# Kernel optimization log

Measured on AMD Instinct MI355X. Metric: run time of the kernel, lower is better.

Reference implementation:

```python
import math
import jax, jax.numpy as jnp
import numpy as np

DIM = 1024
NUM_HEADS = 16
HEAD_DIM = DIM // NUM_HEADS


def setup_inputs() -> dict:
    key = jax.random.key(0)
    ks = jax.random.split(key, 5)
    b, t, d = 2, 2048, DIM
    x = jax.random.normal(ks[0], (b, t, d), dtype=jnp.float32)
    mask = jnp.ones((b, t), dtype=jnp.float32)  # 1 = keep, 0 = pad
    s_in = 1.0 / math.sqrt(d)
    w_qkv = jax.random.normal(ks[1], (3 * d, d), dtype=jnp.float32) * s_in
    b_qkv = jnp.zeros((3 * d,), dtype=jnp.float32)
    w_out = jax.random.normal(ks[2], (d, d), dtype=jnp.float32) * s_in
    b_out = jnp.zeros((d,), dtype=jnp.float32)
    return {"x": x, "mask": mask, "w_qkv": w_qkv, "b_qkv": b_qkv,
            "w_out": w_out, "b_out": b_out}


def reference(x, mask, w_qkv, b_qkv, w_out, b_out):
    b, t, d = x.shape
    h, hd = NUM_HEADS, HEAD_DIM
    # qkv projection (torch Linear: x @ W^T + b)
    qkv = x @ w_qkv.T + b_qkv                          # [b,t,3d]
    q, k, v = jnp.split(qkv, 3, axis=-1)
    def reshape(z):
        return z.reshape(b, t, h, hd).transpose(0, 2, 1, 3)  # [b,h,t,hd]
    q, k, v = reshape(q), reshape(k), reshape(v)
    att = jnp.einsum('bhqd,bhkd->bhqk', q, k) / math.sqrt(hd)  # [b,h,t,t]
    causal = jnp.tril(jnp.ones((t, t), dtype=bool))            # [t,t]
    keep = causal[None, None, :, :] & (mask[:, None, None, :] != 0)
    att = jnp.where(keep, att, -jnp.inf)
    att = jax.nn.softmax(att, axis=-1)
    out = jnp.einsum('bhqk,bhkd->bhqd', att, v)        # [b,h,t,hd]
    out = out.transpose(0, 2, 1, 3).reshape(b, t, d)
    return out @ w_out.T + b_out
```

## Files before the change

kernel.cpp:

```cpp
#include <hip/hip_runtime.h>
#include <cmath>

#define B_ 2
#define T_ 2048
#define D_ 1024
#define H_ 16
#define HD_ 64
#define M_ (B_ * T_)
#define N3_ (3 * D_)
#define K_ 1024

typedef _Float16 halfx8 __attribute__((ext_vector_type(8)));
typedef _Float16 halfx4 __attribute__((ext_vector_type(4)));
typedef _Float16 halfx2 __attribute__((ext_vector_type(2)));
typedef __fp16 fp16x2 __attribute__((ext_vector_type(2)));
typedef float f32x4 __attribute__((ext_vector_type(4)));
typedef float f32x16 __attribute__((ext_vector_type(16)));

#define ASYNC_COPY16(gp, lp) \
  __builtin_amdgcn_global_load_lds((__attribute__((address_space(1))) void*)(gp), \
      (__attribute__((address_space(3))) void*)(lp), 16, 0, 0)

#define QSCALE 0.1803368801111204f
#define RTHR 4.0f

__device__ __forceinline__ float exp2fast(float x) {
#if __has_builtin(__builtin_amdgcn_exp2f)
    return __builtin_amdgcn_exp2f(x);
#else
    return exp2f(x);
#endif
}

__device__ const int QT2_OF[24] = {15,15,7, 14,14, 13,13,6, 12,12, 11,11,5, 10,10, 9,9,4, 8,8, 3,2,1,0};
__device__ const int C2_OF[24]  = { 0, 1,0,  0, 1,  0, 1,0,  0, 1,  0, 1,0,  0, 1, 0,1,0,  0,1, 0,0,0,0};

__global__ __launch_bounds__(256) void prep_all(
    const float* __restrict__ x, const float* __restrict__ wq,
    const float* __restrict__ wo, const float* __restrict__ mask,
    _Float16* __restrict__ xh, _Float16* __restrict__ wqh,
    _Float16* __restrict__ woh, float* __restrict__ kbias,
    int* __restrict__ tflags)
{
    int bid = blockIdx.x;
    if (bid >= 4096) {
        int i = (bid - 4096) * 256 + threadIdx.x;
        float mv = mask[i];
        kbias[i] = (mv != 0.f) ? 0.f : -INFINITY;
        unsigned long long bal = __ballot(mv != 0.f);
        if ((threadIdx.x & 63) == 0) tflags[i >> 6] = (bal == ~0ULL) ? 1 : 0;
        return;
    }
    const float* s; _Float16* d; int off;
    if (bid < 2048)      { s = x;  d = xh;  off = bid; }
    else if (bid < 3584) { s = wq; d = wqh; off = bid - 2048; }
    else                 { s = wo; d = woh; off = bid - 3584; }
    int i = (off * 256 + threadIdx.x) * 8;
    float4 a = *(const float4*)(s + i);
    float4 b = *(const float4*)(s + i + 4);
    halfx8 h;
    h[0] = (_Float16)a.x; h[1] = (_Float16)a.y; h[2] = (_Float16)a.z; h[3] = (_Float16)a.w;
    h[4] = (_Float16)b.x; h[5] = (_Float16)b.y; h[6] = (_Float16)b.z; h[7] = (_Float16)b.w;
    *(halfx8*)(d + i) = h;
}

__global__ __launch_bounds__(256) void gemm_qkv(
    const _Float16* __restrict__ A, const _Float16* __restrict__ Wt,
    const float* __restrict__ bias,
    _Float16* __restrict__ qh, _Float16* __restrict__ kh, _Float16* __restrict__ vth)
{
    __shared__ _Float16 As[128 * 32];
    __shared__ _Float16 Bs[128 * 32];
    const int tid = threadIdx.x;
    const int lane = tid & 63, w = tid >> 6;
    const int col = lane & 15, quad = lane >> 4;
    const int wr = w >> 1, wc = w & 1;
    const int m0 = blockIdx.y << 7, n0 = blockIdx.x << 7;

    const int c0 = w * 2, c1 = c0 + 1;
    const int r0 = c0 * 16 + (lane >> 2), r1 = c1 * 16 + (lane >> 2);
    const int ks = (lane & 3) << 3;

    f32x4 acc[4][4] = {};

    for (int k0 = 0; k0 < K_; k0 += 32) {
        ASYNC_COPY16(A  + (size_t)(m0 + r0) * K_ + k0 + ks, &As[c0 * 512]);
        ASYNC_COPY16(A  + (size_t)(m0 + r1) * K_ + k0 + ks, &As[c1 * 512]);
        ASYNC_COPY16(Wt + (size_t)(n0 + r0) * K_ + k0 + ks, &Bs[c0 * 512]);
        ASYNC_COPY16(Wt + (size_t)(n0 + r1) * K_ + k0 + ks, &Bs[c1 * 512]);
        __syncthreads();
        halfx8 af[4], bf[4];
#pragma unroll
        for (int i = 0; i < 4; ++i)
            af[i] = *(const halfx8*)&As[(wr * 64 + i * 16 + col) * 32 + quad * 8];
#pragma unroll
        for (int j = 0; j < 4; ++j)
            bf[j] = *(const halfx8*)&Bs[(wc * 64 + j * 16 + col) * 32 + quad * 8];
#pragma unroll
        for (int i = 0; i < 4; ++i)
#pragma unroll
            for (int j = 0; j < 4; ++j)
                acc[i][j] = __builtin_amdgcn_mfma_f32_16x16x32_f16(af[i], bf[j], acc[i][j], 0, 0, 0);
        __syncthreads();
    }

#pragma unroll
    for (int i = 0; i < 4; ++i) {
#pragma unroll
        for (int r = 0; r < 4; ++r) {
            int m = m0 + wr * 64 + i * 16 + quad * 4 + r;
            int bb = m >> 11, tt = m & (T_ - 1);
#pragma unroll
            for (int j = 0; j < 4; ++j) {
                int n = n0 + wc * 64 + j * 16 + col;
                float val = acc[i][j][r] + bias[n];
                int which = n >> 10, head = (n >> 6) & 15, dd = n & 63;
                if (which == 0) {
                    qh[((size_t)(bb * H_ + head) * T_ + tt) * HD_ + dd] = (_Float16)(val * QSCALE);
                } else if (which == 1) {
                    int hi = ((dd >> 3) ^ (tt & 7) ^ ((tt >> 3) & 7)) & 7;
                    int dds = (hi << 3) | (dd & 7);
                    kh[((size_t)(bb * H_ + head) * T_ + tt) * HD_ + dds] = (_Float16)val;
                } else {
                    int hi = (((tt >> 3) & 7) ^ (dd & 7) ^ ((dd >> 3) & 7)) & 7;
                    int tts = (tt & ~63) | (hi << 3) | (tt & 7);
                    vth[((size_t)(bb * H_ + head) * HD_ + dd) * T_ + tts] = (_Float16)val;
                }
            }
        }
    }
}

__global__ __launch_bounds__(256) void gemm_out(
    const _Float16* __restrict__ A, const _Float16* __restrict__ Wt,
    const float* __restrict__ bias, float* __restrict__ C)
{
    __shared__ _Float16 As[2][128 * 32];
    __shared__ _Float16 Bs[2][64 * 32];
    const int tid = threadIdx.x;
    const int lane = tid & 63, w = tid >> 6;
    const int col = lane & 15, quad = lane >> 4;
    const int m0 = blockIdx.y << 7, n0 = blockIdx.x << 6;

    const int c0 = w * 2, c1 = c0 + 1;
    const int rA0 = c0 * 16 + (lane >> 2), rA1 = c1 * 16 + (lane >> 2);
    const int rB = w * 16 + (lane >> 2);
    const int ks = (lane & 3) << 3;

    f32x4 acc[2][4] = {};

    for (int k0 = 0; k0 < K_; k0 += 64) {
        ASYNC_COPY16(A  + (size_t)(m0 + rA0) * K_ + k0 + ks,      &As[0][c0 * 512]);
        ASYNC_COPY16(A  + (size_t)(m0 + rA1) * K_ + k0 + ks,      &As[0][c1 * 512]);
        ASYNC_COPY16(A  + (size_t)(m0 + rA0) * K_ + k0 + 32 + ks, &As[1][c0 * 512]);
        ASYNC_COPY16(A  + (size_t)(m0 + rA1) * K_ + k0 + 32 + ks, &As[1][c1 * 512]);
        ASYNC_COPY16(Wt + (size_t)(n0 + rB) * K_ + k0 + ks,       &Bs[0][w * 512]);
        ASYNC_COPY16(Wt + (size_t)(n0 + rB) * K_ + k0 + 32 + ks,  &Bs[1][w * 512]);
        __syncthreads();
#pragma unroll
        for (int half = 0; half < 2; ++half) {
            halfx8 af[2], bf[4];
#pragma unroll
            for (int i = 0; i < 2; ++i)
                af[i] = *(const halfx8*)&As[half][(w * 32 + i * 16 + col) * 32 + quad * 8];
#pragma unroll
            for (int j = 0; j < 4; ++j)
                bf[j] = *(const halfx8*)&Bs[half][(j * 16 + col) * 32 + quad * 8];
#pragma unroll
            for (int i = 0; i < 2; ++i)
#pragma unroll
                for (int j = 0; j < 4; ++j)
                    acc[i][j] = __builtin_amdgcn_mfma_f32_16x16x32_f16(af[i], bf[j], acc[i][j], 0, 0, 0);
        }
        __syncthreads();
    }

#pragma unroll
    for (int i = 0; i < 2; ++i) {
#pragma unroll
        for (int r = 0; r < 4; ++r) {
            int m = m0 + w * 32 + i * 16 + quad * 4 + r;
#pragma unroll
            for (int j = 0; j < 4; ++j) {
                int n = n0 + j * 16 + col;
                C[(size_t)m * D_ + n] = acc[i][j][r] + bias[n];
            }
        }
    }
}

__global__ __launch_bounds__(256, 3) void attn_kernel(
    const _Float16* __restrict__ qh, const _Float16* __restrict__ kh,
    const _Float16* __restrict__ vth, const float* __restrict__ kbias,
    const int* __restrict__ tflags,
    float* __restrict__ pm, float* __restrict__ pl,
    _Float16* __restrict__ po, _Float16* __restrict__ oh)
{
    __shared__ _Float16 Ks[2][64 * 64];
    __shared__ _Float16 Vt[2][64 * 64];

    const int item = blockIdx.x >> 5;
    const int qt = QT2_OF[item], c = C2_OF[item];
    const int hb = blockIdx.x & 31;
    const int h = hb & 15, b = hb >> 4;
    const bool split = (qt >= 8);
    const int tid = threadIdx.x;
    const int lane = tid & 63, w = tid >> 6;
    const int l31 = lane & 31, q2 = lane >> 5;

    const int kt0 = (split && c) ? (qt + 1) : 0;
    const int ktend = (split && !c) ? qt : (2 * qt + 1);

    const int bh = b * H_ + h;
    const _Float16* qp = qh + (size_t)bh * T_ * HD_;
    const _Float16* kp = kh + (size_t)bh * T_ * HD_;
    const _Float16* vp = vth + (size_t)bh * HD_ * T_;
    const float* kb = kbias + (size_t)b * T_;
    const int* tf = tflags + b * 32;

    const int qbase = qt * 128 + w * 32;
    const int q_row = qbase + l31;

    halfx8 bq[4];
#pragma unroll
    for (int hc = 0; hc < 4; ++hc)
        bq[hc] = *(const halfx8*)(qp + (size_t)q_row * HD_ + hc * 16 + q2 * 8);

    float mrow = -INFINITY;
    float lrow = 0.f;
    f32x16 oacc[2] = {};
    const fp16x2 one2 = {(__fp16)1.f, (__fp16)1.f};

    {
        const _Float16* ksrc = kp + (size_t)(kt0 * 64 + w * 16) * HD_;
        ASYNC_COPY16(ksrc + lane * 8, &Ks[0][(w * 16) * 64]);
        ASYNC_COPY16(ksrc + 8 * HD_ + lane * 8, &Ks[0][(w * 16 + 8) * 64]);
        const _Float16* vsrc = vp + (size_t)(w * 16 + (lane >> 3)) * T_
                                 + kt0 * 64 + (lane & 7) * 8;
        ASYNC_COPY16(vsrc, &Vt[0][(w * 16) * 64]);
        ASYNC_COPY16(vsrc + 8 * T_, &Vt[0][(w * 16 + 8) * 64]);
    }

    for (int kt = kt0; kt <= ktend; ++kt) {
        const int cur = (kt - kt0) & 1;
        __syncthreads();
        if (kt < ktend) {
            const int nb = cur ^ 1;
            const _Float16* ksrc = kp + (size_t)((kt + 1) * 64 + w * 16) * HD_;
            ASYNC_COPY16(ksrc + lane * 8, &Ks[nb][(w * 16) * 64]);
            ASYNC_COPY16(ksrc + 8 * HD_ + lane * 8, &Ks[nb][(w * 16 + 8) * 64]);
            const _Float16* vsrc = vp + (size_t)(w * 16 + (lane >> 3)) * T_
                                     + (kt + 1) * 64 + (lane & 7) * 8;
            ASYNC_COPY16(vsrc, &Vt[nb][(w * 16) * 64]);
            ASYNC_COPY16(vsrc + 8 * T_, &Vt[nb][(w * 16 + 8) * 64]);
        }
        if (kt * 64 > qbase + 31) continue;

        const int allkeep = tf[kt];
        const int kb2max = (qbase + 31 - kt * 64 >= 32) ? 2 : 1;

        auto qk_half = [&](int kb2v) -> f32x16 {
            f32x16 a = {};
#pragma unroll
            for (int hc = 0; hc < 4; ++hc) {
                int seg = (hc * 2 + q2) ^ (l31 & 7) ^ ((kb2v * 4 + (l31 >> 3)) & 7);
                halfx8 ka = *(const halfx8*)&Ks[cur][(kb2v * 32 + l31) * 64 + seg * 8];
                a = __builtin_amdgcn_mfma_f32_32x32x16_f16(ka, bq[hc], a, 0, 0, 0);
            }
            return a;
        };
        f32x16 sa0, sa1;
        __builtin_amdgcn_s_setprio(1);
        sa0 = qk_half(0);
        if (kb2max == 2) sa1 = qk_half(1);
        __builtin_amdgcn_s_setprio(0);

        auto smpv = [&](const f32x16& a, int kb2v) {
            float t0 = fmaxf(fmaxf(a[0],  a[1]),  a[2]);
            float t1 = fmaxf(fmaxf(a[3],  a[4]),  a[5]);
            float t2 = fmaxf(fmaxf(a[6],  a[7]),  a[8]);
            float t3 = fmaxf(fmaxf(a[9],  a[10]), a[11]);
            float t4 = fmaxf(fmaxf(a[12], a[13]), a[14]);
            float u0 = fmaxf(fmaxf(t0, t1), t2);
            float u1 = fmaxf(fmaxf(t3, t4), a[15]);
            float mx = fmaxf(u0, u1);

            if (__any(mx > mrow + RTHR)) {
                float mxo = fmaxf(mx, __shfl_xor(mx, 32, 64));
                float mnew = fmaxf(mrow, mxo);
                float alpha = exp2fast(mrow - mnew);
                lrow *= alpha;
#pragma unroll
                for (int db = 0; db < 2; ++db)
#pragma unroll
                    for (int r = 0; r < 16; ++r) oacc[db][r] *= alpha;
                mrow = mnew;
            }

            const bool fastk = allkeep && (kt * 64 + kb2v * 32 + 31 <= qbase);
            halfx4 pf[4];
            float s0 = 0.f, s1 = 0.f;
            if (fastk) {
#pragma unroll
                for (int cc = 0; cc < 4; ++cc) {
                    float e0 = exp2fast(a[cc * 4 + 0] - mrow);
                    float e1 = exp2fast(a[cc * 4 + 1] - mrow);
                    float e2 = exp2fast(a[cc * 4 + 2] - mrow);
                    float e3 = exp2fast(a[cc * 4 + 3] - mrow);
                    fp16x2 lo = __builtin_amdgcn_cvt_pkrtz(e0, e1);
                    fp16x2 hi = __builtin_amdgcn_cvt_pkrtz(e2, e3);
                    halfx2* pfv = (halfx2*)&pf[cc];
                    pfv[0] = __builtin_bit_cast(halfx2, lo);
                    pfv[1] = __builtin_bit_cast(halfx2, hi);
#if __has_builtin(__builtin_amdgcn_fdot2)
                    s0 = __builtin_amdgcn_fdot2(lo, one2, s0, false);
                    s1 = __builtin_amdgcn_fdot2(hi, one2, s1, false);
#else
                    s0 += e0 + e1; s1 += e2 + e3;
#endif
                }
            } else {
#pragma unroll
                for (int cc = 0; cc < 4; ++cc) {
                    float e[4];
#pragma unroll
                    for (int j = 0; j < 4; ++j) {
                        int key = kt * 64 + kb2v * 32 + 8 * cc + 4 * q2 + j;
                        float add = allkeep ? 0.f : kb[key];
                        e[j] = (key <= q_row) ? exp2fast(a[cc * 4 + j] + add - mrow) : 0.f;
                    }
                    fp16x2 lo = __builtin_amdgcn_cvt_pkrtz(e[0], e[1]);
                    fp16x2 hi = __builtin_amdgcn_cvt_pkrtz(e[2], e[3]);
                    halfx2* pfv = (halfx2*)&pf[cc];
                    pfv[0] = __builtin_bit_cast(halfx2, lo);
                    pfv[1] = __builtin_bit_cast(halfx2, hi);
#if __has_builtin(__builtin_amdgcn_fdot2)
                    s0 = __builtin_amdgcn_fdot2(lo, one2, s0, false);
                    s1 = __builtin_amdgcn_fdot2(hi, one2, s1, false);
#else
                    s0 += e[0] + e[1]; s1 += e[2] + e[3];
#endif
                }
            }
            lrow += s0 + s1;

            __builtin_amdgcn_s_setprio(1);
#pragma unroll
            for (int db = 0; db < 2; ++db)
#pragma unroll
                for (int cc = 0; cc < 4; ++cc) {
                    int ck = kb2v * 4 + cc;
                    int seg = ck ^ (l31 & 7) ^ ((db * 4 + (l31 >> 3)) & 7);
                    halfx4 va = *(const halfx4*)&Vt[cur][(db * 32 + l31) * 64 + seg * 8 + q2 * 4];
                    oacc[db] = __builtin_amdgcn_mfma_f32_32x32x8f16(va, pf[cc], oacc[db], 0, 0, 0);
                }
            __builtin_amdgcn_s_setprio(0);
        };

        smpv(sa0, 0);
        if (kb2max == 2) smpv(sa1, 1);
    }

    lrow += __shfl_xor(lrow, 32, 64);

    const int qloc = w * 32 + l31;
    _Float16* ohrow = oh + ((size_t)(b * T_ + qt * 128 + qloc)) * D_ + h * 64;

    if (!split) {
        const float linv = 1.f / lrow;
#pragma unroll
        for (int db = 0; db < 2; ++db)
#pragma unroll
            for (int gg = 0; gg < 4; ++gg) {
                halfx4 ov;
#pragma unroll
                for (int j = 0; j < 4; ++j)
                    ov[j] = (_Float16)(oacc[db][gg * 4 + j] * linv);
                *(halfx4*)(ohrow + db * 32 + 8 * gg + 4 * q2) = ov;
            }
    } else {
        const int slot = (bh * 8 + (qt - 8)) * 2 + c;
        if (q2 == 0) {
            pm[(size_t)slot * 128 + qloc] = mrow;
            pl[(size_t)slot * 128 + qloc] = lrow;
        }
        _Float16* pob = (c == 0) ? ohrow
                      : po + ((size_t)(bh * 8 + (qt - 8)) * 128 + qloc) * 64;
#pragma unroll
        for (int db = 0; db < 2; ++db)
#pragma unroll
            for (int gg = 0; gg < 4; ++gg) {
                halfx4 ov;
#pragma unroll
                for (int j = 0; j < 4; ++j)
                    ov[j] = (_Float16)(oacc[db][gg * 4 + j]);
                *(halfx4*)(pob + db * 32 + 8 * gg + 4 * q2) = ov;
            }
    }
}

__global__ __launch_bounds__(256) void attn_combine(
    const float* __restrict__ pm, const float* __restrict__ pl,
    const _Float16* __restrict__ po, _Float16* __restrict__ oh)
{
    const int qi = blockIdx.x;
    const int h = blockIdx.y, b = blockIdx.z;
    const int bh = b * H_ + h;
    const int tid = threadIdx.x;
    const int r = tid >> 1, dh = tid & 1;

    const int s0 = (bh * 8 + qi) * 2;
    float m0 = pm[(size_t)s0 * 128 + r],       m1 = pm[(size_t)(s0 + 1) * 128 + r];
    float l0 = pl[(size_t)s0 * 128 + r],       l1 = pl[(size_t)(s0 + 1) * 128 + r];
    float ms = fmaxf(m0, m1);
    float w0 = exp2f(m0 - ms), w1 = exp2f(m1 - ms);
    float linv = 1.f / (w0 * l0 + w1 * l1);
    w0 *= linv; w1 *= linv;

    _Float16* ohrow = oh + ((size_t)(b * T_ + (qi + 8) * 128 + r)) * D_ + h * 64 + dh * 32;
    const _Float16* src = po + ((size_t)(bh * 8 + qi) * 128 + r) * 64 + dh * 32;

#pragma unroll
    for (int g = 0; g < 4; ++g) {
        halfx8 o0 = *(const halfx8*)(ohrow + g * 8);
        halfx8 o1 = *(const halfx8*)(src + g * 8);
        halfx8 ov;
#pragma unroll
        for (int j = 0; j < 8; ++j)
            ov[j] = (_Float16)(w0 * (float)o0[j] + w1 * (float)o1[j]);
        *(halfx8*)(ohrow + g * 8) = ov;
    }
}

extern "C" void kernel_launch(void* const* d_in, const int* in_sizes, int n_in,
                              void* d_out, int out_size, void* d_ws, size_t ws_size,
                              hipStream_t stream)
{
    (void)in_sizes; (void)n_in; (void)out_size; (void)ws_size;
    const float* x     = (const float*)d_in[0];
    const float* mask  = (const float*)d_in[1];
    const float* w_qkv = (const float*)d_in[2];
    const float* b_qkv = (const float*)d_in[3];
    const float* w_out = (const float*)d_in[4];
    const float* b_out = (const float*)d_in[5];
    float* out = (float*)d_out;

    const size_t QKV1 = (size_t)B_ * H_ * T_ * HD_;
    _Float16* xh  = (_Float16*)d_ws;
    _Float16* wqh = xh  + (size_t)M_ * K_;
    _Float16* woh = wqh + (size_t)N3_ * K_;
    _Float16* qh  = woh + (size_t)D_ * K_;
    _Float16* kh  = qh  + QKV1;
    _Float16* vth = kh  + QKV1;
    _Float16* oh  = vth + QKV1;
    _Float16* po  = oh  + QKV1;
    float* kbias  = (float*)(po + (size_t)32 * 8 * 128 * 64);
    float* pm     = kbias + (size_t)B_ * T_;
    float* pl     = pm + (size_t)32 * 16 * 128;
    int* tflags   = (int*)(pl + (size_t)32 * 16 * 128);

    prep_all<<<4112, 256, 0, stream>>>(x, w_qkv, w_out, mask,
                                       xh, wqh, woh, kbias, tflags);
    gemm_qkv<<<dim3(N3_ / 128, M_ / 128), 256, 0, stream>>>(
        xh, wqh, b_qkv, qh, kh, vth);
    attn_kernel<<<dim3(768, 1, 1), 256, 0, stream>>>(
        qh, kh, vth, kbias, tflags, pm, pl, po, oh);
    attn_combine<<<dim3(8, H_, B_), 256, 0, stream>>>(
        pm, pl, po, oh);
    gemm_out<<<dim3(D_ / 64, M_ / 128), 256, 0, stream>>>(
        oh, woh, b_out, out);
}
```

Before: 181.7 us.

## Split causal attention KV range into up to three chunks per query tile

Replaces the two-way KV split for the upper query tiles with a table-driven schedule of 37 work items, in which query tiles 3 and up are split into two or three KV chunks of roughly equal length. The combine kernel is extended to merge two or three partial results using their stored max and sum statistics. The aim is to balance per-block work better and give the 256-CU device more blocks in flight. The cost is more partial writes and reads, a heavier combine kernel, and extra per-block table lookups.

```diff
diff --git a/kernel.cpp b/kernel.cpp
--- a/kernel.cpp
+++ b/kernel.cpp
@@ -32,8 +32,22 @@
 #endif
 }
 
-__device__ const int QT2_OF[24] = {15,15,7, 14,14, 13,13,6, 12,12, 11,11,5, 10,10, 9,9,4, 8,8, 3,2,1,0};
-__device__ const int C2_OF[24]  = { 0, 1,0,  0, 1,  0, 1,0,  0, 1,  0, 1,0,  0, 1, 0,1,0,  0,1, 0,0,0,0};
+#define NITEM 37
+#define NPO 21
+__device__ const int QT3_[NITEM] = {
+    15,15, 15,14,14,14,13, 13,13,12,12, 12,11,11,11,10,7,7,
+    10,10,9,9,6,6, 9,8,8,8,5,5,2, 4,4, 3,3,1, 0};
+__device__ const int KT0_[NITEM] = {
+    0,11, 22,0,10,20,0, 10,19,0,9, 18,0,8,16,0,0,8,
+    8,15,0,7,0,7, 14,0,6,12,0,6,0, 0,5, 0,4,0, 0};
+__device__ const int KTE_[NITEM] = {
+    10,21, 31,9,19,29,9, 18,27,8,17, 25,7,15,23,7,7,15,
+    14,21,6,13,6,13, 19,5,11,17,5,11,5, 4,9, 3,7,3, 1};
+__device__ const int C3_[NITEM] = {
+    0,1, 2,0,1,2,0, 1,2,0,1, 2,0,1,2,0,0,1,
+    1,2,0,1,0,1, 2,0,1,2,0,1,0, 0,1, 0,1,0, 0};
+__device__ const int SLOT_BASE[16] = {0,1,2,3,5,7,9,11,13,16,19,22,25,28,31,34};
+__device__ const int PO_BASE[16]   = {0,0,0,0,1,2,3,4,5,7,9,11,13,15,17,19};
 
 __global__ __launch_bounds__(256) void prep_all(
     const float* __restrict__ x, const float* __restrict__ wq,
@@ -200,16 +214,13 @@
     __shared__ _Float16 Vt[2][64 * 64];
 
     const int item = blockIdx.x >> 5;
-    const int qt = QT2_OF[item], c = C2_OF[item];
+    const int qt = QT3_[item], c = C3_[item];
+    const int kt0 = KT0_[item], ktend = KTE_[item];
     const int hb = blockIdx.x & 31;
     const int h = hb & 15, b = hb >> 4;
-    const bool split = (qt >= 8);
     const int tid = threadIdx.x;
     const int lane = tid & 63, w = tid >> 6;
     const int l31 = lane & 31, q2 = lane >> 5;
-
-    const int kt0 = (split && c) ? (qt + 1) : 0;
-    const int ktend = (split && !c) ? qt : (2 * qt + 1);
 
     const int bh = b * H_ + h;
     const _Float16* qp = qh + (size_t)bh * T_ * HD_;
@@ -366,7 +377,7 @@
     const int qloc = w * 32 + l31;
     _Float16* ohrow = oh + ((size_t)(b * T_ + qt * 128 + qloc)) * D_ + h * 64;
 
-    if (!split) {
+    if (qt < 3) {
         const float linv = 1.f / lrow;
 #pragma unroll
         for (int db = 0; db < 2; ++db)
@@ -379,13 +390,13 @@
                 *(halfx4*)(ohrow + db * 32 + 8 * gg + 4 * q2) = ov;
             }
     } else {
-        const int slot = (bh * 8 + (qt - 8)) * 2 + c;
+        const int slot = bh * NITEM + SLOT_BASE[qt] + c;
         if (q2 == 0) {
             pm[(size_t)slot * 128 + qloc] = mrow;
             pl[(size_t)slot * 128 + qloc] = lrow;
         }
         _Float16* pob = (c == 0) ? ohrow
-                      : po + ((size_t)(bh * 8 + (qt - 8)) * 128 + qloc) * 64;
+                      : po + ((size_t)(bh * NPO + PO_BASE[qt] + (c - 1)) * 128 + qloc) * 64;
 #pragma unroll
         for (int db = 0; db < 2; ++db)
 #pragma unroll
@@ -403,31 +414,46 @@
     const float* __restrict__ pm, const float* __restrict__ pl,
     const _Float16* __restrict__ po, _Float16* __restrict__ oh)
 {
-    const int qi = blockIdx.x;
+    const int qt = blockIdx.x + 3;
+    const int nc = (qt >= 8) ? 3 : 2;
     const int h = blockIdx.y, b = blockIdx.z;
     const int bh = b * H_ + h;
     const int tid = threadIdx.x;
     const int r = tid >> 1, dh = tid & 1;
 
-    const int s0 = (bh * 8 + qi) * 2;
-    float m0 = pm[(size_t)s0 * 128 + r],       m1 = pm[(size_t)(s0 + 1) * 128 + r];
-    float l0 = pl[(size_t)s0 * 128 + r],       l1 = pl[(size_t)(s0 + 1) * 128 + r];
-    float ms = fmaxf(m0, m1);
-    float w0 = exp2f(m0 - ms), w1 = exp2f(m1 - ms);
-    float linv = 1.f / (w0 * l0 + w1 * l1);
-    w0 *= linv; w1 *= linv;
-
-    _Float16* ohrow = oh + ((size_t)(b * T_ + (qi + 8) * 128 + r)) * D_ + h * 64 + dh * 32;
-    const _Float16* src = po + ((size_t)(bh * 8 + qi) * 128 + r) * 64 + dh * 32;
+    const int s0 = bh * NITEM + SLOT_BASE[qt];
+    float m0 = pm[(size_t)(s0 + 0) * 128 + r], l0 = pl[(size_t)(s0 + 0) * 128 + r];
+    float m1 = pm[(size_t)(s0 + 1) * 128 + r], l1 = pl[(size_t)(s0 + 1) * 128 + r];
+    float m2 = -INFINITY, l2 = 0.f;
+    if (nc == 3) {
+        m2 = pm[(size_t)(s0 + 2) * 128 + r];
+        l2 = pl[(size_t)(s0 + 2) * 128 + r];
+    }
+    float ms = fmaxf(fmaxf(m0, m1), m2);
+    float w0 = exp2f(m0 - ms), w1 = exp2f(m1 - ms), w2 = exp2f(m2 - ms);
+    float linv = 1.f / (w0 * l0 + w1 * l1 + w2 * l2);
+    w0 *= linv; w1 *= linv; w2 *= linv;
+
+    _Float16* ohrow = oh + ((size_t)(b * T_ + qt * 128 + r)) * D_ + h * 64 + dh * 32;
+    const int pb = bh * NPO + PO_BASE[qt];
+    const _Float16* src1 = po + ((size_t)(pb + 0) * 128 + r) * 64 + dh * 32;
+    const _Float16* src2 = po + ((size_t)(pb + 1) * 128 + r) * 64 + dh * 32;
 
 #pragma unroll
     for (int g = 0; g < 4; ++g) {
         halfx8 o0 = *(const halfx8*)(ohrow + g * 8);
-        halfx8 o1 = *(const halfx8*)(src + g * 8);
+        halfx8 o1 = *(const halfx8*)(src1 + g * 8);
         halfx8 ov;
-#pragma unroll
-        for (int j = 0; j < 8; ++j)
-            ov[j] = (_Float16)(w0 * (float)o0[j] + w1 * (float)o1[j]);
+        if (nc == 3) {
+            halfx8 o2 = *(const halfx8*)(src2 + g * 8);
+#pragma unroll
+            for (int j = 0; j < 8; ++j)
+                ov[j] = (_Float16)(w0 * (float)o0[j] + w1 * (float)o1[j] + w2 * (float)o2[j]);
+        } else {
+#pragma unroll
+            for (int j = 0; j < 8; ++j)
+                ov[j] = (_Float16)(w0 * (float)o0[j] + w1 * (float)o1[j]);
+        }
         *(halfx8*)(ohrow + g * 8) = ov;
     }
 }
@@ -454,18 +480,18 @@
     _Float16* vth = kh  + QKV1;
     _Float16* oh  = vth + QKV1;
     _Float16* po  = oh  + QKV1;
-    float* kbias  = (float*)(po + (size_t)32 * 8 * 128 * 64);
+    float* kbias  = (float*)(po + (size_t)32 * NPO * 128 * 64);
     float* pm     = kbias + (size_t)B_ * T_;
-    float* pl     = pm + (size_t)32 * 16 * 128;
-    int* tflags   = (int*)(pl + (size_t)32 * 16 * 128);
+    float* pl     = pm + (size_t)32 * NITEM * 128;
+    int* tflags   = (int*)(pl + (size_t)32 * NITEM * 128);
 
     prep_all<<<4112, 256, 0, stream>>>(x, w_qkv, w_out, mask,
                                        xh, wqh, woh, kbias, tflags);
     gemm_qkv<<<dim3(N3_ / 128, M_ / 128), 256, 0, stream>>>(
         xh, wqh, b_qkv, qh, kh, vth);
-    attn_kernel<<<dim3(768, 1, 1), 256, 0, stream>>>(
+    attn_kernel<<<dim3(NITEM * 32, 1, 1), 256, 0, stream>>>(
         qh, kh, vth, kbias, tflags, pm, pl, po, oh);
-    attn_combine<<<dim3(8, H_, B_), 256, 0, stream>>>(
+    attn_combine<<<dim3(13, H_, B_), 256, 0, stream>>>(
         pm, pl, po, oh);
     gemm_out<<<dim3(D_ / 64, M_ / 128), 256, 0, stream>>>(
         oh, woh, b_out, out);
```

After: 187.0 us. 3.0% more time.
